# Kernel tuning notes

Hardware: AMD Instinct MI355X
Metric: run time of the kernel (lower is better)

## Reference

```python
import jax, jax.numpy as jnp
import numpy as np

B, N, T, K = 2, 128, 1000, 30
L, S, R, DC = 4, 12, 8, 4  # layers, d_state, dt_rank, d_conv


def _ln(x, w, b, eps=1e-5):
    m = jnp.mean(x, -1, keepdims=True)
    v = jnp.var(x, -1, keepdims=True)
    return (x - m) * jax.lax.rsqrt(v + eps) * w + b


def setup_inputs():
    key = jax.random.key(0)
    ks = jax.random.split(key, 10)
    n = lambda k, shp, s=0.05: jax.random.normal(k, shp, jnp.float32) * s
    return {
        "x": jax.random.normal(ks[0], (B, N, T, K), jnp.float32),
        "ln_w": jnp.ones((L, N), jnp.float32),
        "ln_b": jnp.zeros((L, N), jnp.float32),
        "in_w": n(ks[1], (L, 2 * N, N)),
        "in_b": jnp.zeros((L, 2 * N), jnp.float32),
        "conv_w": n(ks[2], (L, N, DC), 0.3),
        "conv_b": jnp.zeros((L, N), jnp.float32),
        "xp_w": n(ks[3], (L, R + 2 * S, N)),
        "dtp_w": n(ks[4], (L, N, R)),
        "dtp_b": n(ks[5], (L, N), 0.5),
        "A_log": jnp.log(jnp.tile(jnp.arange(1.0, S + 1.0, dtype=jnp.float32), (L, N, 1))),
        "Dv": jnp.ones((L, N), jnp.float32),
        "out_w": n(ks[6], (L, N, N)),
        "out_b": jnp.zeros((L, N), jnp.float32),
        "cb_w": n(ks[7], (N, N), 0.09),
        "cb_b": jnp.zeros((N,), jnp.float32),
        "cb_ln_w": jnp.ones((N,), jnp.float32),
        "cb_ln_b": jnp.zeros((N,), jnp.float32),
        "fin_ln_w": jnp.ones((N,), jnp.float32),
        "fin_ln_b": jnp.zeros((N,), jnp.float32),
    }


def _mamba_block(seq, p):
    # seq: [BK, T, N]; canonical Mamba-1 block with pre-LN and residual
    lnw, lnb, iw, ib, cw, cb, xw, dw, db, alog, dv, ow, ob = p
    x = _ln(seq, lnw, lnb)
    xz = x @ iw.T + ib                         # [BK,T,2N]
    xc, z = jnp.split(xz, 2, axis=-1)
    # causal depthwise conv, kernel size DC
    xp = jnp.pad(xc, ((0, 0), (DC - 1, 0), (0, 0)))
    Tlen = xc.shape[1]
    conv = sum(xp[:, k:k + Tlen, :] * cw[:, k] for k in range(DC))
    xc = jax.nn.silu(conv + cb)
    dbc = xc @ xw.T                            # [BK,T,R+2S]
    dt = jax.nn.softplus(dbc[..., :R] @ dw.T + db)  # [BK,T,N]
    Bm = dbc[..., R:R + S]                     # [BK,T,S]
    Cm = dbc[..., R + S:]                      # [BK,T,S]
    A = -jnp.exp(alog)                         # [N,S]

    def step(h, inp):
        dt_t, B_t, C_t, x_t = inp              # [BK,N],[BK,S],[BK,S],[BK,N]
        dA = jnp.exp(dt_t[..., None] * A)      # [BK,N,S]
        h = dA * h + dt_t[..., None] * B_t[:, None, :] * x_t[..., None]
        y = jnp.einsum('bns,bs->bn', h, C_t)
        return h, y

    h0 = jnp.zeros((xc.shape[0], xc.shape[2], S), xc.dtype)
    xs = (jnp.swapaxes(dt, 0, 1), jnp.swapaxes(Bm, 0, 1),
          jnp.swapaxes(Cm, 0, 1), jnp.swapaxes(xc, 0, 1))
    _, ys = jax.lax.scan(step, h0, xs)
    y = jnp.swapaxes(ys, 0, 1) + dv * xc
    y = y * jax.nn.silu(z)
    return y @ ow.T + ob + seq


def reference(x, ln_w, ln_b, in_w, in_b, conv_w, conv_b, xp_w, dtp_w, dtp_b,
              A_log, Dv, out_w, out_b, cb_w, cb_b, cb_ln_w, cb_ln_b, fin_ln_w, fin_ln_b):
    b, n, t, k = x.shape
    seq = jnp.transpose(x, (0, 3, 2, 1)).reshape(b * k, t, n)  # [BK,T,N]

    def lstep(s, p):
        return _mamba_block(s, p), None

    seq, _ = jax.lax.scan(lstep, seq, (ln_w, ln_b, in_w, in_b, conv_w, conv_b,
                                       xp_w, dtp_w, dtp_b, A_log, Dv, out_w, out_b))
    main = jnp.transpose(seq.reshape(b, k, t, n), (0, 2, 1, 3))  # [B,T,K,N]
    cross = jax.nn.gelu(_ln(main @ cb_w.T + cb_b, cb_ln_w, cb_ln_b), approximate=False)
    feat = _ln(main + cross, fin_ln_w, fin_ln_b)
    return jnp.transpose(feat, (0, 3, 1, 2))  # [B,N,T,K]
```

## Files before the change

### kernel.cpp

```cpp
#include <hip/hip_runtime.h>
#include <math.h>

#define BKS 60
#define TL  1000
#define NF  128
#define SD  12
#define RD  8
#define NCH 32
#define CLEN 32
#define NTOK (BKS*TL)
#define MT  64
#define NBLK ((NTOK + MT - 1)/MT)
#define LNP 129
#define OFF_OW  131072
#define OFF_CBW 196608
#define OFF_XW  212992
#define WCNT    229376

typedef __bf16 bf16x8 __attribute__((ext_vector_type(8)));
typedef float  f32x4  __attribute__((ext_vector_type(4)));

__device__ __forceinline__ float siluf(float x){ return x / (1.f + __expf(-x)); }
__device__ __forceinline__ float softplusf(float x){
  if (x > 20.f) return x;
  float e = __expf(x);
  return (x < -20.f) ? e : __logf(1.f + e);
}
__device__ __forceinline__ ushort bf16r(float f){
  uint u = __float_as_uint(f);
  return (ushort)((u + 0x7FFFu + ((u>>16)&1u)) >> 16);
}
__device__ __forceinline__ float bf2f(ushort h){ return __uint_as_float(((uint)h)<<16); }

__global__ __launch_bounds__(256) void k_ingest(const float* __restrict__ x, float* __restrict__ seq){
  const int b = blockIdx.x / TL, t = blockIdx.x % TL;
  __shared__ float tile[30*NF];
  for (int e = threadIdx.x; e < 30*NF; e += 256){
    int n = e / 30, k = e - n*30;
    tile[k*NF + n] = x[((size_t)(b*NF + n)*TL + t)*30 + k];
  }
  __syncthreads();
  const size_t base = ((size_t)b*30)*TL*NF + (size_t)t*NF;
  for (int e = threadIdx.x; e < 30*NF; e += 256){
    int k = e >> 7, n = e & 127;
    seq[base + (size_t)k*TL*NF + n] = tile[e];
  }
}

__global__ __launch_bounds__(256) void k_wconv(
    const float* __restrict__ iw, const float* __restrict__ ow,
    const float* __restrict__ cw, const float* __restrict__ xw,
    ushort* __restrict__ wh, ushort* __restrict__ wl){
  const int idx = blockIdx.x*256 + threadIdx.x;
  if (idx >= WCNT) return;
  float v;
  if (idx < OFF_OW)       v = iw[idx];
  else if (idx < OFF_CBW) v = ow[idx - OFF_OW];
  else if (idx < OFF_XW)  v = cw[idx - OFF_CBW];
  else                    v = xw[idx - OFF_XW];
  const ushort h = bf16r(v);
  wh[idx] = h;
  wl[idx] = bf16r(v - bf2f(h));
}

__global__ __launch_bounds__(256) void k_ln_inproj(
    const float* __restrict__ seq, const float* __restrict__ lnw, const float* __restrict__ lnb,
    const ushort* __restrict__ wh, const ushort* __restrict__ wl, const float* __restrict__ ib,
    float* __restrict__ xcr, float* __restrict__ zb){
  __shared__ short xsh[MT*NF];
  __shared__ short xsl[MT*NF];
  const int tid = threadIdx.x;
  const int tok0 = blockIdx.x * MT;

  {
    const int j = tid >> 4, l16 = tid & 15;
    const float4 w0 = *(const float4*)(lnw + l16*8);
    const float4 w1 = *(const float4*)(lnw + l16*8 + 4);
    const float4 b0 = *(const float4*)(lnb + l16*8);
    const float4 b1 = *(const float4*)(lnb + l16*8 + 4);
    const float lw[8] = {w0.x,w0.y,w0.z,w0.w, w1.x,w1.y,w1.z,w1.w};
    const float lb[8] = {b0.x,b0.y,b0.z,b0.w, b1.x,b1.y,b1.z,b1.w};
    for (int it = 0; it < 4; ++it){
      const int t = j + 16*it;
      const int tok = tok0 + t;
      float v[8]; float s = 0.f, s2 = 0.f;
      if (tok < NTOK){
        const float* sp = seq + (size_t)tok*NF + l16*8;
        const float4 a0 = *(const float4*)sp;
        const float4 a1 = *(const float4*)(sp + 4);
        v[0]=a0.x; v[1]=a0.y; v[2]=a0.z; v[3]=a0.w;
        v[4]=a1.x; v[5]=a1.y; v[6]=a1.z; v[7]=a1.w;
        #pragma unroll
        for (int i = 0; i < 8; ++i){ s += v[i]; s2 += v[i]*v[i]; }
      } else {
        #pragma unroll
        for (int i = 0; i < 8; ++i) v[i] = 0.f;
      }
      #pragma unroll
      for (int m = 1; m < 16; m <<= 1){ s += __shfl_xor(s, m, 64); s2 += __shfl_xor(s2, m, 64); }
      const float mean = s * (1.f/128.f);
      const float rstd = rsqrtf(s2*(1.f/128.f) - mean*mean + 1e-5f);
      const int swz = (t & 7) << 3;
      const int nb = (l16*8) ^ swz;
      ushort hs[8], ls[8];
      #pragma unroll
      for (int i = 0; i < 8; ++i){
        const float f = (v[i]-mean)*rstd*lw[i] + lb[i];
        const ushort h = bf16r(f);
        hs[i] = h;
        ls[i] = bf16r(f - bf2f(h));
      }
      uint4 hv, lv;
      hv.x = (uint)hs[0] | ((uint)hs[1] << 16); hv.y = (uint)hs[2] | ((uint)hs[3] << 16);
      hv.z = (uint)hs[4] | ((uint)hs[5] << 16); hv.w = (uint)hs[6] | ((uint)hs[7] << 16);
      lv.x = (uint)ls[0] | ((uint)ls[1] << 16); lv.y = (uint)ls[2] | ((uint)ls[3] << 16);
      lv.z = (uint)ls[4] | ((uint)ls[5] << 16); lv.w = (uint)ls[6] | ((uint)ls[7] << 16);
      *(uint4*)&xsh[t*NF + nb] = hv;
      *(uint4*)&xsl[t*NF + nb] = lv;
    }
  }
  __syncthreads();

  const int w = tid >> 6, lane = tid & 63;
  const int cl = lane & 15, q8 = (lane >> 4) * 8;
  const int obase = w * 64;
  f32x4 acc[4][4];
  #pragma unroll
  for (int m = 0; m < 4; ++m)
    #pragma unroll
    for (int nt = 0; nt < 4; ++nt) acc[m][nt] = (f32x4){0.f,0.f,0.f,0.f};

  for (int c = 0; c < 4; ++c){
    bf16x8 ah[4], al[4];
    #pragma unroll
    for (int m = 0; m < 4; ++m){
      const int r = m*16 + cl;
      const int hi = r*NF + ((c*32 + q8) ^ ((r & 7) << 3));
      ah[m] = *(const bf16x8*)&xsh[hi];
      al[m] = *(const bf16x8*)&xsl[hi];
    }
    #pragma unroll
    for (int nt = 0; nt < 4; ++nt){
      const int o = obase + nt*16 + cl;
      const size_t wo = (size_t)o*NF + c*32 + q8;
      const bf16x8 bh = *(const bf16x8*)(wh + wo);
      const bf16x8 bl = *(const bf16x8*)(wl + wo);
      #pragma unroll
      for (int m = 0; m < 4; ++m){
        acc[m][nt] = __builtin_amdgcn_mfma_f32_16x16x32_bf16(ah[m], bh, acc[m][nt], 0, 0, 0);
        acc[m][nt] = __builtin_amdgcn_mfma_f32_16x16x32_bf16(al[m], bh, acc[m][nt], 0, 0, 0);
        acc[m][nt] = __builtin_amdgcn_mfma_f32_16x16x32_bf16(ah[m], bl, acc[m][nt], 0, 0, 0);
      }
    }
  }

  const int rbase = (lane >> 4) * 4;
  #pragma unroll
  for (int nt = 0; nt < 4; ++nt){
    const int o = obase + nt*16 + cl;
    const float bias = ib[o];
    float* dst = (o < NF) ? xcr : zb;
    const int oc = (o < NF) ? o : (o - NF);
    #pragma unroll
    for (int m = 0; m < 4; ++m)
      #pragma unroll
      for (int j2 = 0; j2 < 4; ++j2){
        const int tok = tok0 + m*16 + rbase + j2;
        if (tok < NTOK) dst[(size_t)tok*NF + oc] = acc[m][nt][j2] + bias;
      }
  }
}

__global__ __launch_bounds__(256) void k_conv_scan1(
    const float* __restrict__ xcr,
    const float* __restrict__ cw, const float* __restrict__ cb,
    const ushort* __restrict__ xwh, const ushort* __restrict__ xwl,
    const float* __restrict__ dw, const float* __restrict__ db,
    const float* __restrict__ alog,
    float* __restrict__ xcc, float* __restrict__ dtb,
    float* __restrict__ Bmb, float* __restrict__ Cmb,
    float* __restrict__ ap, float* __restrict__ hfb){
  __shared__ float smem[9600];
  float* sxr  = smem;
  float* sdt  = smem;
  short* xch  = (short*)(smem + 4480);
  short* xcl  = (short*)(smem + 6528);
  float* sdbc = smem + 8576;
  const int bid = blockIdx.x;
  const int sq = bid / NCH, cblk = bid - sq*NCH;
  const int t0 = cblk*CLEN;
  const int lim = (TL - t0 < CLEN) ? (TL - t0) : CLEN;
  const int tid = threadIdx.x;

  for (int i = 0; i < 5; ++i){
    const int e4 = tid + i*256;
    if (e4 < 35*32){
      const int r = e4 >> 5, n4 = (e4 & 31) << 2;
      const int t = t0 - 3 + r;
      float4 v = make_float4(0.f,0.f,0.f,0.f);
      if (t >= 0 && t < TL) v = *(const float4*)(xcr + ((size_t)sq*TL + t)*NF + n4);
      *(float4*)(sxr + r*NF + n4) = v;
    }
  }
  __syncthreads();

  #pragma unroll
  for (int i = 0; i < 4; ++i){
    const int e4 = tid + i*256;
    const int r = e4 >> 5, n4 = (e4 & 31) << 2;
    const float4 c0 = *(const float4*)(cw + (size_t)(n4+0)*4);
    const float4 c1 = *(const float4*)(cw + (size_t)(n4+1)*4);
    const float4 c2 = *(const float4*)(cw + (size_t)(n4+2)*4);
    const float4 c3 = *(const float4*)(cw + (size_t)(n4+3)*4);
    const float4 x0 = *(const float4*)(sxr + (r+0)*NF + n4);
    const float4 x1 = *(const float4*)(sxr + (r+1)*NF + n4);
    const float4 x2 = *(const float4*)(sxr + (r+2)*NF + n4);
    const float4 x3 = *(const float4*)(sxr + (r+3)*NF + n4);
    float4 a = *(const float4*)(cb + n4);
    a.x = fmaf(x3.x, c0.w, fmaf(x2.x, c0.z, fmaf(x1.x, c0.y, fmaf(x0.x, c0.x, a.x))));
    a.y = fmaf(x3.y, c1.w, fmaf(x2.y, c1.z, fmaf(x1.y, c1.y, fmaf(x0.y, c1.x, a.y))));
    a.z = fmaf(x3.z, c2.w, fmaf(x2.z, c2.z, fmaf(x1.z, c2.y, fmaf(x0.z, c2.x, a.z))));
    a.w = fmaf(x3.w, c3.w, fmaf(x2.w, c3.z, fmaf(x1.w, c3.y, fmaf(x0.w, c3.x, a.w))));
    a.x = siluf(a.x); a.y = siluf(a.y); a.z = siluf(a.z); a.w = siluf(a.w);
    const ushort h0 = bf16r(a.x), h1 = bf16r(a.y), h2 = bf16r(a.z), h3 = bf16r(a.w);
    const ushort l0 = bf16r(a.x - bf2f(h0)), l1 = bf16r(a.y - bf2f(h1));
    const ushort l2 = bf16r(a.z - bf2f(h2)), l3 = bf16r(a.w - bf2f(h3));
    const int bi = r*NF + (n4 ^ ((r & 7) << 3));
    *(uint2*)&xch[bi] = make_uint2((uint)h0 | ((uint)h1 << 16), (uint)h2 | ((uint)h3 << 16));
    *(uint2*)&xcl[bi] = make_uint2((uint)l0 | ((uint)l1 << 16), (uint)l2 | ((uint)l3 << 16));
    if (r < lim) *(float4*)(xcc + ((size_t)sq*TL + t0 + r)*NF + n4) = a;
  }
  __syncthreads();

  {
    const int w = tid >> 6, lane = tid & 63;
    const int cl = lane & 15, q8 = (lane >> 4) * 8;
    const int m = w & 1, nt = w >> 1;
    f32x4 acc = (f32x4){0.f,0.f,0.f,0.f};
    for (int c = 0; c < 4; ++c){
      const int r = m*16 + cl;
      const int ai = r*NF + ((c*32 + q8) ^ ((r & 7) << 3));
      const bf16x8 ah = *(const bf16x8*)&xch[ai];
      const bf16x8 al = *(const bf16x8*)&xcl[ai];
      const int o = nt*16 + cl;
      const size_t wo = (size_t)o*NF + c*32 + q8;
      const bf16x8 bh = *(const bf16x8*)(xwh + wo);
      const bf16x8 bl = *(const bf16x8*)(xwl + wo);
      acc = __builtin_amdgcn_mfma_f32_16x16x32_bf16(ah, bh, acc, 0, 0, 0);
      acc = __builtin_amdgcn_mfma_f32_16x16x32_bf16(al, bh, acc, 0, 0, 0);
      acc = __builtin_amdgcn_mfma_f32_16x16x32_bf16(ah, bl, acc, 0, 0, 0);
    }
    const int rb = m*16 + (lane >> 4)*4;
    const int o = nt*16 + cl;
    #pragma unroll
    for (int j = 0; j < 4; ++j)
      sdbc[(rb + j)*32 + o] = acc[j];
  }
  __syncthreads();

  #pragma unroll
  for (int i = 0; i < 16; ++i){
    const int e = tid + i*256;
    const int r = e >> 7, n = e & 127;
    const float4 b0 = *(const float4*)(sdbc + r*32);
    const float4 b1 = *(const float4*)(sdbc + r*32 + 4);
    const float4 w0 = *(const float4*)(dw + (size_t)n*8);
    const float4 w1 = *(const float4*)(dw + (size_t)n*8 + 4);
    float acc = db[n];
    acc = fmaf(b0.x, w0.x, acc); acc = fmaf(b0.y, w0.y, acc);
    acc = fmaf(b0.z, w0.z, acc); acc = fmaf(b0.w, w0.w, acc);
    acc = fmaf(b1.x, w1.x, acc); acc = fmaf(b1.y, w1.y, acc);
    acc = fmaf(b1.z, w1.z, acc); acc = fmaf(b1.w, w1.w, acc);
    const float dtv = softplusf(acc);
    sdt[e] = dtv;
    if (e < lim*NF) dtb[((size_t)sq*TL + t0)*NF + e] = dtv;
  }
  for (int e = tid; e < CLEN*2*SD; e += 256){
    int r = e / (2*SD), c = e - r*2*SD;
    if (r < lim){
      float v = sdbc[r*32 + 8 + c];
      size_t tok = (size_t)sq*TL + t0 + r;
      if (c < SD) Bmb[tok*SD + c] = v;
      else        Cmb[tok*SD + (c - SD)] = v;
    }
  }
  __syncthreads();

  {
    const int n = tid & 127, p = tid >> 7;
    float Av[6], h[6];
    #pragma unroll
    for (int s = 0; s < 6; ++s){
      Av[s] = -__expf(alog[(size_t)n*SD + p*6 + s]);
      h[s] = 0.f;
    }
    bool fast = true;
    #pragma unroll
    for (int s = 0; s < 6; ++s)
      fast = fast && (fabsf(Av[s] + (float)(p*6 + s + 1)) <= 1e-3f);
    float dts = 0.f;
    if (fast){
      for (int tt = 0; tt < lim; ++tt){
        const float dtv = sdt[tt*NF + n];
        const int xi = tt*NF + (n ^ ((tt & 7) << 3));
        const float xcv = bf2f((ushort)xch[xi]) + bf2f((ushort)xcl[xi]);
        float Bv[6];
        const float* br = sdbc + tt*32 + 8 + p*6;
        if (p == 0){
          const float4 a = *(const float4*)br;
          const float2 b = *(const float2*)(br + 4);
          Bv[0]=a.x; Bv[1]=a.y; Bv[2]=a.z; Bv[3]=a.w; Bv[4]=b.x; Bv[5]=b.y;
        } else {
          const float2 a = *(const float2*)br;
          const float4 b = *(const float4*)(br + 2);
          Bv[0]=a.x; Bv[1]=a.y; Bv[2]=b.x; Bv[3]=b.y; Bv[4]=b.z; Bv[5]=b.w;
        }
        const float dx = dtv * xcv;
        dts += dtv;
        const float q = __expf(-dtv);
        float dA;
        if (p == 0) dA = q;
        else { const float q2 = q*q; const float q4 = q2*q2; dA = q4*q2*q; }
        h[0] = fmaf(dA, h[0], dx*Bv[0]);
        #pragma unroll
        for (int s = 1; s < 6; ++s){ dA *= q; h[s] = fmaf(dA, h[s], dx*Bv[s]); }
      }
    } else {
      for (int tt = 0; tt < lim; ++tt){
        const float dtv = sdt[tt*NF + n];
        const int xi = tt*NF + (n ^ ((tt & 7) << 3));
        const float xcv = bf2f((ushort)xch[xi]) + bf2f((ushort)xcl[xi]);
        float Bv[6];
        const float* br = sdbc + tt*32 + 8 + p*6;
        if (p == 0){
          const float4 a = *(const float4*)br;
          const float2 b = *(const float2*)(br + 4);
          Bv[0]=a.x; Bv[1]=a.y; Bv[2]=a.z; Bv[3]=a.w; Bv[4]=b.x; Bv[5]=b.y;
        } else {
          const float2 a = *(const float2*)br;
          const float4 b = *(const float4*)(br + 2);
          Bv[0]=a.x; Bv[1]=a.y; Bv[2]=b.x; Bv[3]=b.y; Bv[4]=b.z; Bv[5]=b.w;
        }
        const float dx = dtv * xcv;
        dts += dtv;
        #pragma unroll
        for (int s = 0; s < 6; ++s){
          const float dA = __expf(dtv*Av[s]);
          h[s] = fmaf(dA, h[s], dx*Bv[s]);
        }
      }
    }
    const size_t base = (size_t)bid*SD*NF + n;
    #pragma unroll
    for (int s = 0; s < 6; ++s){
      ap [base + (p*6+s)*NF] = __expf(Av[s]*dts);
      hfb[base + (p*6+s)*NF] = h[s];
    }
  }
}

__global__ __launch_bounds__(128) void k_scan_combine(
    const float* __restrict__ ap, const float* __restrict__ hfb, float* __restrict__ hinit){
  const int sq = blockIdx.x;
  const int n = threadIdx.x;
  float h[SD];
  #pragma unroll
  for (int s = 0; s < SD; ++s) h[s] = 0.f;
  for (int c = 0; c < NCH; ++c){
    const size_t base = ((size_t)sq*NCH + c)*SD*NF + n;
    #pragma unroll
    for (int s = 0; s < SD; ++s){
      hinit[base + s*NF] = h[s];
      h[s] = fmaf(ap[base + s*NF], h[s], hfb[base + s*NF]);
    }
  }
}

__global__ __launch_bounds__(128) void k_scan_pass2(
    const float* __restrict__ dtb, const float* __restrict__ xcc,
    const float* __restrict__ Bmb, const float* __restrict__ Cmb,
    const float* __restrict__ alog, const float* __restrict__ hinit,
    const float* __restrict__ zb, const float* __restrict__ Dv,
    float* __restrict__ yb){
  const int bid = blockIdx.x;
  const int sq = bid / NCH, c = bid - sq*NCH;
  const int t0 = c*CLEN;
  const int lim = (TL - t0 < CLEN) ? (TL - t0) : CLEN;
  const int n = threadIdx.x;
  const float4* A4 = (const float4*)(alog + (size_t)n*SD);
  float4 Aa = A4[0], Ab = A4[1], Ac = A4[2];
  float Av[SD] = {Aa.x,Aa.y,Aa.z,Aa.w, Ab.x,Ab.y,Ab.z,Ab.w, Ac.x,Ac.y,Ac.z,Ac.w};
  #pragma unroll
  for (int s = 0; s < SD; ++s) Av[s] = -__expf(Av[s]);
  bool fast = true;
  #pragma unroll
  for (int s = 0; s < SD; ++s)
    fast = fast && (fabsf(Av[s] + (float)(s + 1)) <= 1e-3f);
  const float dvn = Dv[n];
  float h[SD];
  const size_t hbase = (size_t)bid*SD*NF + n;
  #pragma unroll
  for (int s = 0; s < SD; ++s) h[s] = hinit[hbase + s*NF];
  const size_t tok0 = (size_t)sq*TL + t0;
  if (fast){
    for (int tt = 0; tt < lim; ++tt){
      const size_t tok = tok0 + tt;
      float dtv = dtb[tok*NF + n];
      float xcv = xcc[tok*NF + n];
      float dx  = dtv * xcv;
      const float4* B4 = (const float4*)(Bmb + tok*SD);
      const float4* C4 = (const float4*)(Cmb + tok*SD);
      float4 Ba=B4[0], Bb=B4[1], Bc=B4[2];
      float4 Ca=C4[0], Cb=C4[1], Cc=C4[2];
      float Bv[SD] = {Ba.x,Ba.y,Ba.z,Ba.w, Bb.x,Bb.y,Bb.z,Bb.w, Bc.x,Bc.y,Bc.z,Bc.w};
      float Cv[SD] = {Ca.x,Ca.y,Ca.z,Ca.w, Cb.x,Cb.y,Cb.z,Cb.w, Cc.x,Cc.y,Cc.z,Cc.w};
      const float q = __expf(-dtv);
      float dA = q;
      float yv = 0.f;
      h[0] = fmaf(dA, h[0], dx*Bv[0]);
      yv = fmaf(h[0], Cv[0], yv);
      #pragma unroll
      for (int s = 1; s < SD; ++s){
        dA *= q;
        h[s] = fmaf(dA, h[s], dx*Bv[s]);
        yv = fmaf(h[s], Cv[s], yv);
      }
      float zv = zb[tok*NF + n];
      yb[tok*NF + n] = fmaf(dvn, xcv, yv) * siluf(zv);
    }
  } else {
    for (int tt = 0; tt < lim; ++tt){
      const size_t tok = tok0 + tt;
      float dtv = dtb[tok*NF + n];
      float xcv = xcc[tok*NF + n];
      float dx  = dtv * xcv;
      const float4* B4 = (const float4*)(Bmb + tok*SD);
      const float4* C4 = (const float4*)(Cmb + tok*SD);
      float4 Ba=B4[0], Bb=B4[1], Bc=B4[2];
      float4 Ca=C4[0], Cb=C4[1], Cc=C4[2];
      float Bv[SD] = {Ba.x,Ba.y,Ba.z,Ba.w, Bb.x,Bb.y,Bb.z,Bb.w, Bc.x,Bc.y,Bc.z,Bc.w};
      float Cv[SD] = {Ca.x,Ca.y,Ca.z,Ca.w, Cb.x,Cb.y,Cb.z,Cb.w, Cc.x,Cc.y,Cc.z,Cc.w};
      float yv = 0.f;
      #pragma unroll
      for (int s = 0; s < SD; ++s){
        float dA = __expf(dtv*Av[s]);
        h[s] = fmaf(dA, h[s], dx*Bv[s]);
        yv = fmaf(h[s], Cv[s], yv);
      }
      float zv = zb[tok*NF + n];
      yb[tok*NF + n] = fmaf(dvn, xcv, yv) * siluf(zv);
    }
  }
}

__global__ __launch_bounds__(256) void k_gate_out(
    const float* __restrict__ yb,
    const ushort* __restrict__ wh, const ushort* __restrict__ wl, const float* __restrict__ ob,
    float* __restrict__ seq){
  __shared__ short xsh[MT*NF];
  __shared__ short xsl[MT*NF];
  const int tid = threadIdx.x;
  const int tok0 = blockIdx.x * MT;

  #pragma unroll
  for (int i = 0; i < 8; ++i){
    const int r  = (tid & 15) + ((i & 3) << 4);
    const int nq = (tid >> 4) + ((i >> 2) << 4);
    const int tok = tok0 + r;
    float4 v = make_float4(0.f,0.f,0.f,0.f);
    if (tok < NTOK) v = *(const float4*)(yb + (size_t)tok*NF + nq*4);
    const ushort h0 = bf16r(v.x), h1 = bf16r(v.y), h2 = bf16r(v.z), h3 = bf16r(v.w);
    const ushort l0 = bf16r(v.x - bf2f(h0)), l1 = bf16r(v.y - bf2f(h1));
    const ushort l2 = bf16r(v.z - bf2f(h2)), l3 = bf16r(v.w - bf2f(h3));
    const int hi = r*NF + ((nq*4) ^ ((r & 7) << 3));
    *(uint2*)&xsh[hi] = make_uint2((uint)h0 | ((uint)h1 << 16), (uint)h2 | ((uint)h3 << 16));
    *(uint2*)&xsl[hi] = make_uint2((uint)l0 | ((uint)l1 << 16), (uint)l2 | ((uint)l3 << 16));
  }
  __syncthreads();

  const int w = tid >> 6, lane = tid & 63;
  const int cl = lane & 15, q8 = (lane >> 4) * 8;
  const int obase = w * 32;
  f32x4 acc[4][2];
  #pragma unroll
  for (int m = 0; m < 4; ++m)
    #pragma unroll
    for (int nt = 0; nt < 2; ++nt) acc[m][nt] = (f32x4){0.f,0.f,0.f,0.f};

  for (int c = 0; c < 4; ++c){
    bf16x8 ah[4], al[4];
    #pragma unroll
    for (int m = 0; m < 4; ++m){
      const int r = m*16 + cl;
      const int hi = r*NF + ((c*32 + q8) ^ ((r & 7) << 3));
      ah[m] = *(const bf16x8*)&xsh[hi];
      al[m] = *(const bf16x8*)&xsl[hi];
    }
    #pragma unroll
    for (int nt = 0; nt < 2; ++nt){
      const int o = obase + nt*16 + cl;
      const size_t wo = (size_t)o*NF + c*32 + q8;
      const bf16x8 bh = *(const bf16x8*)(wh + wo);
      const bf16x8 bl = *(const bf16x8*)(wl + wo);
      #pragma unroll
      for (int m = 0; m < 4; ++m){
        acc[m][nt] = __builtin_amdgcn_mfma_f32_16x16x32_bf16(ah[m], bh, acc[m][nt], 0, 0, 0);
        acc[m][nt] = __builtin_amdgcn_mfma_f32_16x16x32_bf16(al[m], bh, acc[m][nt], 0, 0, 0);
        acc[m][nt] = __builtin_amdgcn_mfma_f32_16x16x32_bf16(ah[m], bl, acc[m][nt], 0, 0, 0);
      }
    }
  }

  const int rbase = (lane >> 4) * 4;
  #pragma unroll
  for (int nt = 0; nt < 2; ++nt){
    const int o = obase + nt*16 + cl;
    const float bias = ob[o];
    #pragma unroll
    for (int m = 0; m < 4; ++m)
      #pragma unroll
      for (int j2 = 0; j2 < 4; ++j2){
        const int tok = tok0 + m*16 + rbase + j2;
        if (tok < NTOK){
          float* dst = seq + (size_t)tok*NF + o;
          *dst = *dst + acc[m][nt][j2] + bias;
        }
      }
  }
}

__global__ __launch_bounds__(256) void k_cross_gemm(
    const float* __restrict__ seq,
    const ushort* __restrict__ wh, const ushort* __restrict__ wl, const float* __restrict__ cbb,
    float* __restrict__ cross){
  __shared__ short xsh[MT*NF];
  __shared__ short xsl[MT*NF];
  const int tid = threadIdx.x;
  const int tok0 = blockIdx.x * MT;

  #pragma unroll
  for (int i = 0; i < 8; ++i){
    const int r  = (tid & 15) + ((i & 3) << 4);
    const int nq = (tid >> 4) + ((i >> 2) << 4);
    const int tok = tok0 + r;
    float4 v = make_float4(0.f,0.f,0.f,0.f);
    if (tok < NTOK){
      int b = tok / 30000, rr = tok - b*30000;
      int t = rr / 30, k = rr - t*30;
      v = *(const float4*)(seq + ((size_t)(b*30 + k)*TL + t)*NF + nq*4);
    }
    const ushort h0 = bf16r(v.x), h1 = bf16r(v.y), h2 = bf16r(v.z), h3 = bf16r(v.w);
    const ushort l0 = bf16r(v.x - bf2f(h0)), l1 = bf16r(v.y - bf2f(h1));
    const ushort l2 = bf16r(v.z - bf2f(h2)), l3 = bf16r(v.w - bf2f(h3));
    const int hi = r*NF + ((nq*4) ^ ((r & 7) << 3));
    *(uint2*)&xsh[hi] = make_uint2((uint)h0 | ((uint)h1 << 16), (uint)h2 | ((uint)h3 << 16));
    *(uint2*)&xsl[hi] = make_uint2((uint)l0 | ((uint)l1 << 16), (uint)l2 | ((uint)l3 << 16));
  }
  __syncthreads();

  const int w = tid >> 6, lane = tid & 63;
  const int cl = lane & 15, q8 = (lane >> 4) * 8;
  const int obase = w * 32;
  f32x4 acc[4][2];
  #pragma unroll
  for (int m = 0; m < 4; ++m)
    #pragma unroll
    for (int nt = 0; nt < 2; ++nt) acc[m][nt] = (f32x4){0.f,0.f,0.f,0.f};

  for (int c = 0; c < 4; ++c){
    bf16x8 ah[4], al[4];
    #pragma unroll
    for (int m = 0; m < 4; ++m){
      const int r = m*16 + cl;
      const int hi = r*NF + ((c*32 + q8) ^ ((r & 7) << 3));
      ah[m] = *(const bf16x8*)&xsh[hi];
      al[m] = *(const bf16x8*)&xsl[hi];
    }
    #pragma unroll
    for (int nt = 0; nt < 2; ++nt){
      const int o = obase + nt*16 + cl;
      const size_t wo = (size_t)o*NF + c*32 + q8;
      const bf16x8 bh = *(const bf16x8*)(wh + wo);
      const bf16x8 bl = *(const bf16x8*)(wl + wo);
      #pragma unroll
      for (int m = 0; m < 4; ++m){
        acc[m][nt] = __builtin_amdgcn_mfma_f32_16x16x32_bf16(ah[m], bh, acc[m][nt], 0, 0, 0);
        acc[m][nt] = __builtin_amdgcn_mfma_f32_16x16x32_bf16(al[m], bh, acc[m][nt], 0, 0, 0);
        acc[m][nt] = __builtin_amdgcn_mfma_f32_16x16x32_bf16(ah[m], bl, acc[m][nt], 0, 0, 0);
      }
    }
  }

  const int rbase = (lane >> 4) * 4;
  #pragma unroll
  for (int nt = 0; nt < 2; ++nt){
    const int o = obase + nt*16 + cl;
    const float bias = cbb[o];
    #pragma unroll
    for (int m = 0; m < 4; ++m)
      #pragma unroll
      for (int j2 = 0; j2 < 4; ++j2){
        const int tok = tok0 + m*16 + rbase + j2;
        if (tok < NTOK) cross[(size_t)tok*NF + o] = acc[m][nt][j2] + bias;
      }
  }
}

__global__ __launch_bounds__(256) void k_cross_ln(
    const float* __restrict__ seq, const float* __restrict__ cross,
    const float* __restrict__ clnw, const float* __restrict__ clnb,
    const float* __restrict__ flnw, const float* __restrict__ flnb,
    float* __restrict__ out){
  __shared__ float fs[32*LNP];
  const int tid = threadIdx.x;
  const int tok0 = blockIdx.x * 32;
  const int j16 = tid >> 4, l16 = tid & 15;

  for (int it = 0; it < 2; ++it){
    const int jj = j16 + 16*it;
    const int tok = tok0 + jj;
    const int b = tok / 30000, rr = tok - b*30000;
    const int t = rr / 30, k = rr - t*30;
    const float* cp = cross + (size_t)tok*NF;
    const float* mp = seq + ((size_t)(b*30 + k)*TL + t)*NF;
    float cv[8]; float s = 0.f, s2 = 0.f;
    #pragma unroll
    for (int i = 0; i < 8; ++i){
      float f = cp[l16 + 16*i]; cv[i] = f; s += f; s2 += f*f;
    }
    #pragma unroll
    for (int m = 1; m < 16; m <<= 1){ s += __shfl_xor(s, m, 64); s2 += __shfl_xor(s2, m, 64); }
    float mu = s * (1.f/128.f);
    float rs = rsqrtf(s2*(1.f/128.f) - mu*mu + 1e-5f);
    float rv[8]; float rsum = 0.f, rsum2 = 0.f;
    #pragma unroll
    for (int i = 0; i < 8; ++i){
      int n = l16 + 16*i;
      float cn = (cv[i] - mu)*rs*clnw[n] + clnb[n];
      float g = 0.5f*cn*(1.f + erff(cn*0.70710678118f));
      float res = mp[n] + g;
      rv[i] = res; rsum += res; rsum2 += res*res;
    }
    #pragma unroll
    for (int m = 1; m < 16; m <<= 1){ rsum += __shfl_xor(rsum, m, 64); rsum2 += __shfl_xor(rsum2, m, 64); }
    float mu2 = rsum * (1.f/128.f);
    float rs2 = rsqrtf(rsum2*(1.f/128.f) - mu2*mu2 + 1e-5f);
    #pragma unroll
    for (int i = 0; i < 8; ++i){
      int n = l16 + 16*i;
      fs[jj*LNP + n] = (rv[i] - mu2)*rs2*flnw[n] + flnb[n];
    }
  }
  __syncthreads();

  #pragma unroll
  for (int i = 0; i < 16; ++i){
    const int e = tid + i*256;
    const int j = e & 31, n = e >> 5;
    const int tok = tok0 + j;
    const int b = tok / 30000, rr = tok - b*30000;
    out[(size_t)(b*NF + n)*30000 + rr] = fs[j*LNP + n];
  }
}

extern "C" void kernel_launch(void* const* d_in, const int* in_sizes, int n_in,
                              void* d_out, int out_size, void* d_ws, size_t ws_size,
                              hipStream_t stream){
  const float* x       = (const float*)d_in[0];
  const float* ln_w    = (const float*)d_in[1];
  const float* ln_b    = (const float*)d_in[2];
  const float* in_w    = (const float*)d_in[3];
  const float* in_b    = (const float*)d_in[4];
  const float* conv_w  = (const float*)d_in[5];
  const float* conv_b  = (const float*)d_in[6];
  const float* xp_w    = (const float*)d_in[7];
  const float* dtp_w   = (const float*)d_in[8];
  const float* dtp_b   = (const float*)d_in[9];
  const float* A_log   = (const float*)d_in[10];
  const float* Dv      = (const float*)d_in[11];
  const float* out_w   = (const float*)d_in[12];
  const float* out_b   = (const float*)d_in[13];
  const float* cb_w    = (const float*)d_in[14];
  const float* cb_b    = (const float*)d_in[15];
  const float* cb_ln_w = (const float*)d_in[16];
  const float* cb_ln_b = (const float*)d_in[17];
  const float* fin_ln_w= (const float*)d_in[18];
  const float* fin_ln_b= (const float*)d_in[19];
  float* out = (float*)d_out;

  const size_t SEQSZ = (size_t)BKS*TL*NF;
  const size_t CHSZ  = (size_t)BKS*NF*NCH*SD;
  const size_t FBASE = 6*SEQSZ + 2*(size_t)BKS*TL*SD;
  const size_t BASE  = FBASE + WCNT;
  float* ws  = (float*)d_ws;
  float* seq = ws;
  float* xcr = ws + SEQSZ;
  float* zb  = ws + 2*SEQSZ;
  float* xcc = ws + 3*SEQSZ;
  float* dtb = ws + 4*SEQSZ;
  float* yb  = ws + 5*SEQSZ;
  float* Bmb = ws + 6*SEQSZ;
  float* Cmb = Bmb + (size_t)BKS*TL*SD;
  ushort* wbh = (ushort*)(ws + FBASE);
  ushort* wbl = wbh + WCNT;
  if (ws_size < BASE*sizeof(float)) return;

  float* ap    = yb;
  float* hfb   = yb + CHSZ;
  float* hinit = xcr;
  float* cross = dtb;

  k_wconv<<<(WCNT + 255)/256, 256, 0, stream>>>(in_w, out_w, cb_w, xp_w, wbh, wbl);
  k_ingest<<<2*TL, 256, 0, stream>>>(x, seq);
  for (int l = 0; l < 4; ++l){
    k_ln_inproj<<<NBLK, 256, 0, stream>>>(seq, ln_w + l*NF, ln_b + l*NF,
        wbh + (size_t)l*32768, wbl + (size_t)l*32768, in_b + l*2*NF, xcr, zb);
    k_conv_scan1<<<BKS*NCH, 256, 0, stream>>>(xcr, conv_w + (size_t)l*NF*4, conv_b + l*NF,
        wbh + OFF_XW + (size_t)l*4096, wbl + OFF_XW + (size_t)l*4096,
        dtp_w + (size_t)l*NF*RD, dtp_b + l*NF,
        A_log + (size_t)l*NF*SD, xcc, dtb, Bmb, Cmb, ap, hfb);
    k_scan_combine<<<BKS, NF, 0, stream>>>(ap, hfb, hinit);
    k_scan_pass2<<<BKS*NCH, NF, 0, stream>>>(dtb, xcc, Bmb, Cmb, A_log + (size_t)l*NF*SD,
        hinit, zb, Dv + l*NF, yb);
    k_gate_out<<<NBLK, 256, 0, stream>>>(yb,
        wbh + OFF_OW + (size_t)l*16384, wbl + OFF_OW + (size_t)l*16384, out_b + l*NF, seq);
  }
  k_cross_gemm<<<NBLK, 256, 0, stream>>>(seq, wbh + OFF_CBW, wbl + OFF_CBW, cb_b, cross);
  k_cross_ln<<<NTOK/32, 256, 0, stream>>>(seq, cross, cb_ln_w, cb_ln_b, fin_ln_w, fin_ln_b, out);
}
```

Before: 729.2 us.

## Fuse out-projection residual with next layer's LayerNorm and in-projection

Adds a k_gate_ln kernel that computes the out-projection GEMM and residual update for layer l, keeps the resulting token rows in shared memory, and applies the next layer's LayerNorm and in-projection GEMM in the same block. This removes three of the four separate k_ln_inproj launches and the global re-read of seq between layers. The fused kernel uses more shared memory (64x132 floats) and more registers, which may reduce occupancy, and the extra syncs serialize the stages within each block.

```diff
diff --git a/kernel.cpp b/kernel.cpp
--- a/kernel.cpp
+++ b/kernel.cpp
@@ -12,6 +12,7 @@
 #define MT  64
 #define NBLK ((NTOK + MT - 1)/MT)
 #define LNP 129
+#define SQP 132
 #define OFF_OW  131072
 #define OFF_CBW 196608
 #define OFF_XW  212992
@@ -529,6 +530,194 @@
   }
 }
 
+__global__ __launch_bounds__(256) void k_gate_ln(
+    const float* __restrict__ yb,
+    const ushort* __restrict__ gwh, const ushort* __restrict__ gwl, const float* __restrict__ ob,
+    const float* __restrict__ lnw, const float* __restrict__ lnb,
+    const ushort* __restrict__ iwh, const ushort* __restrict__ iwl, const float* __restrict__ ib,
+    float* __restrict__ seq, float* __restrict__ xcr, float* __restrict__ zb){
+  __shared__ float smem[MT*SQP];
+  short* xsh = (short*)smem;
+  short* xsl = xsh + MT*NF;
+  float* sqf = smem;
+  const int tid = threadIdx.x;
+  const int tok0 = blockIdx.x * MT;
+
+  #pragma unroll
+  for (int i = 0; i < 8; ++i){
+    const int r  = (tid & 15) + ((i & 3) << 4);
+    const int nq = (tid >> 4) + ((i >> 2) << 4);
+    const int tok = tok0 + r;
+    float4 v = make_float4(0.f,0.f,0.f,0.f);
+    if (tok < NTOK) v = *(const float4*)(yb + (size_t)tok*NF + nq*4);
+    const ushort h0 = bf16r(v.x), h1 = bf16r(v.y), h2 = bf16r(v.z), h3 = bf16r(v.w);
+    const ushort l0 = bf16r(v.x - bf2f(h0)), l1 = bf16r(v.y - bf2f(h1));
+    const ushort l2 = bf16r(v.z - bf2f(h2)), l3 = bf16r(v.w - bf2f(h3));
+    const int hi = r*NF + ((nq*4) ^ ((r & 7) << 3));
+    *(uint2*)&xsh[hi] = make_uint2((uint)h0 | ((uint)h1 << 16), (uint)h2 | ((uint)h3 << 16));
+    *(uint2*)&xsl[hi] = make_uint2((uint)l0 | ((uint)l1 << 16), (uint)l2 | ((uint)l3 << 16));
+  }
+  __syncthreads();
+
+  const int w = tid >> 6, lane = tid & 63;
+  const int cl = lane & 15, q8 = (lane >> 4) * 8;
+  {
+    const int obase = w * 32;
+    f32x4 acc[4][2];
+    #pragma unroll
+    for (int m = 0; m < 4; ++m)
+      #pragma unroll
+      for (int nt = 0; nt < 2; ++nt) acc[m][nt] = (f32x4){0.f,0.f,0.f,0.f};
+
+    for (int c = 0; c < 4; ++c){
+      bf16x8 ah[4], al[4];
+      #pragma unroll
+      for (int m = 0; m < 4; ++m){
+        const int r = m*16 + cl;
+        const int hi = r*NF + ((c*32 + q8) ^ ((r & 7) << 3));
+        ah[m] = *(const bf16x8*)&xsh[hi];
+        al[m] = *(const bf16x8*)&xsl[hi];
+      }
+      #pragma unroll
+      for (int nt = 0; nt < 2; ++nt){
+        const int o = obase + nt*16 + cl;
+        const size_t wo = (size_t)o*NF + c*32 + q8;
+        const bf16x8 bh = *(const bf16x8*)(gwh + wo);
+        const bf16x8 bl = *(const bf16x8*)(gwl + wo);
+        #pragma unroll
+        for (int m = 0; m < 4; ++m){
+          acc[m][nt] = __builtin_amdgcn_mfma_f32_16x16x32_bf16(ah[m], bh, acc[m][nt], 0, 0, 0);
+          acc[m][nt] = __builtin_amdgcn_mfma_f32_16x16x32_bf16(al[m], bh, acc[m][nt], 0, 0, 0);
+          acc[m][nt] = __builtin_amdgcn_mfma_f32_16x16x32_bf16(ah[m], bl, acc[m][nt], 0, 0, 0);
+        }
+      }
+    }
+    __syncthreads();
+
+    const int rbase = (lane >> 4) * 4;
+    #pragma unroll
+    for (int nt = 0; nt < 2; ++nt){
+      const int o = obase + nt*16 + cl;
+      const float bias = ob[o];
+      #pragma unroll
+      for (int m = 0; m < 4; ++m)
+        #pragma unroll
+        for (int j2 = 0; j2 < 4; ++j2){
+          const int lt = m*16 + rbase + j2;
+          const int tok = tok0 + lt;
+          float sv = 0.f;
+          if (tok < NTOK){
+            float* dst = seq + (size_t)tok*NF + o;
+            sv = *dst + acc[m][nt][j2] + bias;
+            *dst = sv;
+          }
+          sqf[lt*SQP + o] = sv;
+        }
+    }
+  }
+  __syncthreads();
+
+  {
+    const int j = tid >> 4, l16 = tid & 15;
+    const float4 w0 = *(const float4*)(lnw + l16*8);
+    const float4 w1 = *(const float4*)(lnw + l16*8 + 4);
+    const float4 b0 = *(const float4*)(lnb + l16*8);
+    const float4 b1 = *(const float4*)(lnb + l16*8 + 4);
+    const float lw[8] = {w0.x,w0.y,w0.z,w0.w, w1.x,w1.y,w1.z,w1.w};
+    const float lb[8] = {b0.x,b0.y,b0.z,b0.w, b1.x,b1.y,b1.z,b1.w};
+    float outv[4][8];
+    #pragma unroll
+    for (int it = 0; it < 4; ++it){
+      const int t = j + 16*it;
+      const float* rp = sqf + t*SQP + l16*8;
+      float v[8]; float s = 0.f, s2 = 0.f;
+      const float4 a0 = *(const float4*)rp;
+      const float4 a1 = *(const float4*)(rp + 4);
+      v[0]=a0.x; v[1]=a0.y; v[2]=a0.z; v[3]=a0.w;
+      v[4]=a1.x; v[5]=a1.y; v[6]=a1.z; v[7]=a1.w;
+      #pragma unroll
+      for (int i = 0; i < 8; ++i){ s += v[i]; s2 += v[i]*v[i]; }
+      #pragma unroll
+      for (int m = 1; m < 16; m <<= 1){ s += __shfl_xor(s, m, 64); s2 += __shfl_xor(s2, m, 64); }
+      const float mean = s * (1.f/128.f);
+      const float rstd = rsqrtf(s2*(1.f/128.f) - mean*mean + 1e-5f);
+      #pragma unroll
+      for (int i = 0; i < 8; ++i)
+        outv[it][i] = (v[i]-mean)*rstd*lw[i] + lb[i];
+    }
+    __syncthreads();
+    #pragma unroll
+    for (int it = 0; it < 4; ++it){
+      const int t = j + 16*it;
+      const int nb = (l16*8) ^ ((t & 7) << 3);
+      ushort hs[8], ls[8];
+      #pragma unroll
+      for (int i = 0; i < 8; ++i){
+        const ushort h = bf16r(outv[it][i]);
+        hs[i] = h;
+        ls[i] = bf16r(outv[it][i] - bf2f(h));
+      }
+      uint4 hv, lv;
+      hv.x = (uint)hs[0] | ((uint)hs[1] << 16); hv.y = (uint)hs[2] | ((uint)hs[3] << 16);
+      hv.z = (uint)hs[4] | ((uint)hs[5] << 16); hv.w = (uint)hs[6] | ((uint)hs[7] << 16);
+      lv.x = (uint)ls[0] | ((uint)ls[1] << 16); lv.y = (uint)ls[2] | ((uint)ls[3] << 16);
+      lv.z = (uint)ls[4] | ((uint)ls[5] << 16); lv.w = (uint)ls[6] | ((uint)ls[7] << 16);
+      *(uint4*)&xsh[t*NF + nb] = hv;
+      *(uint4*)&xsl[t*NF + nb] = lv;
+    }
+  }
+  __syncthreads();
+
+  {
+    const int obase = w * 64;
+    f32x4 acc[4][4];
+    #pragma unroll
+    for (int m = 0; m < 4; ++m)
+      #pragma unroll
+      for (int nt = 0; nt < 4; ++nt) acc[m][nt] = (f32x4){0.f,0.f,0.f,0.f};
+
+    for (int c = 0; c < 4; ++c){
+      bf16x8 ah[4], al[4];
+      #pragma unroll
+      for (int m = 0; m < 4; ++m){
+        const int r = m*16 + cl;
+        const int hi = r*NF + ((c*32 + q8) ^ ((r & 7) << 3));
+        ah[m] = *(const bf16x8*)&xsh[hi];
+        al[m] = *(const bf16x8*)&xsl[hi];
+      }
+      #pragma unroll
+      for (int nt = 0; nt < 4; ++nt){
+        const int o = obase + nt*16 + cl;
+        const size_t wo = (size_t)o*NF + c*32 + q8;
+        const bf16x8 bh = *(const bf16x8*)(iwh + wo);
+        const bf16x8 bl = *(const bf16x8*)(iwl + wo);
+        #pragma unroll
+        for (int m = 0; m < 4; ++m){
+          acc[m][nt] = __builtin_amdgcn_mfma_f32_16x16x32_bf16(ah[m], bh, acc[m][nt], 0, 0, 0);
+          acc[m][nt] = __builtin_amdgcn_mfma_f32_16x16x32_bf16(al[m], bh, acc[m][nt], 0, 0, 0);
+          acc[m][nt] = __builtin_amdgcn_mfma_f32_16x16x32_bf16(ah[m], bl, acc[m][nt], 0, 0, 0);
+        }
+      }
+    }
+
+    const int rbase = (lane >> 4) * 4;
+    #pragma unroll
+    for (int nt = 0; nt < 4; ++nt){
+      const int o = obase + nt*16 + cl;
+      const float bias = ib[o];
+      float* dst = (o < NF) ? xcr : zb;
+      const int oc = (o < NF) ? o : (o - NF);
+      #pragma unroll
+      for (int m = 0; m < 4; ++m)
+        #pragma unroll
+        for (int j2 = 0; j2 < 4; ++j2){
+          const int tok = tok0 + m*16 + rbase + j2;
+          if (tok < NTOK) dst[(size_t)tok*NF + oc] = acc[m][nt][j2] + bias;
+        }
+    }
+  }
+}
+
 __global__ __launch_bounds__(256) void k_cross_gemm(
     const float* __restrict__ seq,
     const ushort* __restrict__ wh, const ushort* __restrict__ wl, const float* __restrict__ cbb,
@@ -712,9 +901,8 @@
 
   k_wconv<<<(WCNT + 255)/256, 256, 0, stream>>>(in_w, out_w, cb_w, xp_w, wbh, wbl);
   k_ingest<<<2*TL, 256, 0, stream>>>(x, seq);
+  k_ln_inproj<<<NBLK, 256, 0, stream>>>(seq, ln_w, ln_b, wbh, wbl, in_b, xcr, zb);
   for (int l = 0; l < 4; ++l){
-    k_ln_inproj<<<NBLK, 256, 0, stream>>>(seq, ln_w + l*NF, ln_b + l*NF,
-        wbh + (size_t)l*32768, wbl + (size_t)l*32768, in_b + l*2*NF, xcr, zb);
     k_conv_scan1<<<BKS*NCH, 256, 0, stream>>>(xcr, conv_w + (size_t)l*NF*4, conv_b + l*NF,
         wbh + OFF_XW + (size_t)l*4096, wbl + OFF_XW + (size_t)l*4096,
         dtp_w + (size_t)l*NF*RD, dtp_b + l*NF,
@@ -722,8 +910,16 @@
     k_scan_combine<<<BKS, NF, 0, stream>>>(ap, hfb, hinit);
     k_scan_pass2<<<BKS*NCH, NF, 0, stream>>>(dtb, xcc, Bmb, Cmb, A_log + (size_t)l*NF*SD,
         hinit, zb, Dv + l*NF, yb);
-    k_gate_out<<<NBLK, 256, 0, stream>>>(yb,
-        wbh + OFF_OW + (size_t)l*16384, wbl + OFF_OW + (size_t)l*16384, out_b + l*NF, seq);
+    if (l < 3){
+      k_gate_ln<<<NBLK, 256, 0, stream>>>(yb,
+          wbh + OFF_OW + (size_t)l*16384, wbl + OFF_OW + (size_t)l*16384, out_b + l*NF,
+          ln_w + (l+1)*NF, ln_b + (l+1)*NF,
+          wbh + (size_t)(l+1)*32768, wbl + (size_t)(l+1)*32768, in_b + (l+1)*2*NF,
+          seq, xcr, zb);
+    } else {
+      k_gate_out<<<NBLK, 256, 0, stream>>>(yb,
+          wbh + OFF_OW + (size_t)l*16384, wbl + OFF_OW + (size_t)l*16384, out_b + l*NF, seq);
+    }
   }
   k_cross_gemm<<<NBLK, 256, 0, stream>>>(seq, wbh + OFF_CBW, wbl + OFF_CBW, cb_b, cross);
   k_cross_ln<<<NTOK/32, 256, 0, stream>>>(seq, cross, cb_ln_w, cb_ln_b, fin_ln_w, fin_ln_b, out);
```

Result: slower. 772.7 us (+6.0%).
